# Kernel tuning notes

Hardware: AMD Instinct MI355X
Metric: run time of the kernel (lower is better)

Reference implementation:

```python
import jax, jax.numpy as jnp
import numpy as np

B, Nc, Ns, Nz, Nx, K = 2, 128, 2048, 256, 256, 4


def setup_inputs() -> dict:
    key = jax.random.key(0)
    k1, k2, k3 = jax.random.split(key, 3)
    # RF channel data: [B, Nc, Ns, K]
    rf = jax.random.normal(k1, (B, Nc, Ns, K), dtype=jnp.float32)
    # Imaging grid point coordinates (meters), ~4 cm field: [B, Nz, Nx, 3]
    g = jax.random.uniform(k2, (B, Nz, Nx, 3), dtype=jnp.float32) * 0.04
    # Receiver element positions (meters): [B, Nc, 3]
    pr = jax.random.uniform(k3, (B, Nc, 3), dtype=jnp.float32) * 0.04
    # Acquisition params per batch: [c0 (m/s), fs (Hz), t0 (s), unused]
    p = jnp.tile(jnp.array([1540.0, 40.0e6, 0.0, 0.0], dtype=jnp.float32), (B, 1))
    return {"rf": rf, "g": g, "pr": pr, "p": p}


def reference(rf, g, pr, p):
    # rf: [B, Nc, Ns, K]; g: [B, Nz, Nx, 3]; pr: [B, Nc, 3]; p: [B, 4]
    b, nc, ns, k = rf.shape
    nz, nx = g.shape[1], g.shape[2]
    m = nz * nx

    c0 = p[:, 0][:, None, None, None]
    fs = p[:, 1][:, None, None, None]
    t0 = p[:, 2][:, None, None, None]

    d_tx = g[..., 2]  # [B, Nz, Nx] transmit path = depth coordinate
    # receive path: distance from each receiver to each pixel -> [B, Nc, Nz, Nx]
    d_rx = jnp.linalg.norm(g[:, None, :, :, :] - pr[:, :, None, None, :], axis=-1)
    # fractional sample index of the round-trip delay
    samples = fs * (t0 + (d_rx + d_tx[:, None, :, :])) / c0  # [B, Nc, Nz, Nx]
    s = samples.reshape(b, nc, m)

    # batch_interp_regular_1d_grid with x_ref_min=0, x_ref_max=Ns-1 on Ns points
    # -> unit grid spacing, constant extension (clamp) outside the grid.
    s = jnp.clip(s, 0.0, float(ns - 1))
    i0 = jnp.clip(jnp.floor(s).astype(jnp.int32), 0, ns - 2)  # [B, Nc, M]
    w = (s - i0.astype(s.dtype))[..., None]                   # [B, Nc, M, 1]

    idx0 = jnp.broadcast_to(i0[..., None], (b, nc, m, k))
    y0 = jnp.take_along_axis(rf, idx0, axis=2)      # [B, Nc, M, K]
    y1 = jnp.take_along_axis(rf, idx0 + 1, axis=2)  # [B, Nc, M, K]
    interp = y0 * (1.0 - w) + y1 * w

    # delay-and-sum over channels, then back to image layout [B, Nz, Nx, K]
    y_das = jnp.sum(interp, axis=1).reshape(b, nz, nx, k)
    return y_das
```

## Files before the change

### kernel.cpp

```cpp
#include <hip/hip_runtime.h>


#define NBATCH 2
#define NC 128
#define NS 2048
#define NK 4
#define NM 65536

#define THREADS 1024
#define PX_PER_THREAD 2
#define PX_PER_BLOCK (THREADS * PX_PER_THREAD)
#define C_PER_BLOCK 16
#define N_CHUNKS (NC / C_PER_BLOCK)
#define N_TILES (NM / PX_PER_BLOCK)
#define NBLOCKS (NBATCH * N_TILES * N_CHUNKS)
#define SLICE_F4 (NS * NK / 4)

#define PART_BYTES ((size_t)N_CHUNKS * NBATCH * NM * NK * 4)

__device__ __forceinline__ void stage_channel(const float* slice, float4* lbuf, int t) {
#pragma unroll
    for (int r = 0; r < SLICE_F4 / THREADS; ++r) {
        const int d = r * THREADS + t;
        __builtin_amdgcn_global_load_lds(
            (const __attribute__((address_space(1))) void*)(slice + (size_t)d * 4),
            (__attribute__((address_space(3))) void*)(lbuf + d),
            16, 0, 0);
    }
}

template <bool ATOMIC>
__global__ __launch_bounds__(THREADS, 8) void das_kernel(
    const float* __restrict__ rf, const float* __restrict__ g,
    const float* __restrict__ pr, const float* __restrict__ p,
    float* __restrict__ dst)
{
    __shared__ float4 sbuf[2][SLICE_F4];

    const int bid   = blockIdx.x;
    const int chunk = bid & (N_CHUNKS - 1);
    const int tile  = (bid >> 3) & (N_TILES - 1);
    const int b     = bid >> 8;
    const int t     = threadIdx.x;
    const int px0   = tile * PX_PER_BLOCK;

    const float c0v = p[b * 4 + 0];
    const float fsv = p[b * 4 + 1];
    const float t0v = p[b * 4 + 2];
    const float scale = fsv / c0v;
    const float sb0   = scale * t0v;

    float gx[PX_PER_THREAD], gy[PX_PER_THREAD], gzv[PX_PER_THREAD], sbase[PX_PER_THREAD];
#pragma unroll
    for (int j = 0; j < PX_PER_THREAD; ++j) {
        const int m = px0 + j * THREADS + t;
        const float* gp = g + ((size_t)b * NM + m) * 3;
        gx[j]  = gp[0];
        gy[j]  = gp[1];
        gzv[j] = gp[2];
        sbase[j] = sb0 + scale * gzv[j];
    }

    float4 acc[PX_PER_THREAD];
#pragma unroll
    for (int j = 0; j < PX_PER_THREAD; ++j) acc[j] = make_float4(0.f, 0.f, 0.f, 0.f);

    const int ch0 = chunk * C_PER_BLOCK;
    const float* slice0 = rf + (size_t)(b * NC + ch0) * NS * NK;

    stage_channel(slice0, &sbuf[0][0], t);

    for (int cc = 0; cc < C_PER_BLOCK; ++cc) {
        __syncthreads();
        if (cc + 1 < C_PER_BLOCK)
            stage_channel(slice0 + (size_t)(cc + 1) * NS * NK,
                          &sbuf[(cc + 1) & 1][0], t);

        const float4* lb = &sbuf[cc & 1][0];
        const float* prp = pr + ((size_t)(b * NC + ch0 + cc)) * 3;
        const float prx = prp[0], pry = prp[1], prz = prp[2];

#pragma unroll
        for (int j = 0; j < PX_PER_THREAD; ++j) {
            const float dx = gx[j]  - prx;
            const float dy = gy[j]  - pry;
            const float dz = gzv[j] - prz;
            const float drx = __builtin_amdgcn_sqrtf(fmaf(dx, dx, fmaf(dy, dy, dz * dz)));
            float s = fmaf(scale, drx, sbase[j]);
            s = fminf(fmaxf(s, 0.0f), (float)(NS - 1));
            const float fi = fminf(floorf(s), (float)(NS - 2));
            const float w  = s - fi;
            const float wm = 1.0f - w;
            const int i0 = (int)fi;
            const float4 y0 = lb[i0];
            const float4 y1 = lb[i0 + 1];
            acc[j].x = fmaf(y0.x, wm, fmaf(y1.x, w, acc[j].x));
            acc[j].y = fmaf(y0.y, wm, fmaf(y1.y, w, acc[j].y));
            acc[j].z = fmaf(y0.z, wm, fmaf(y1.z, w, acc[j].z));
            acc[j].w = fmaf(y0.w, wm, fmaf(y1.w, w, acc[j].w));
        }
    }

    if (ATOMIC) {
        float* ob = dst + (size_t)b * NM * NK;
#pragma unroll
        for (int j = 0; j < PX_PER_THREAD; ++j) {
            const int m = px0 + j * THREADS + t;
            float* op = ob + (size_t)m * NK;
            atomicAdd(op + 0, acc[j].x);
            atomicAdd(op + 1, acc[j].y);
            atomicAdd(op + 2, acc[j].z);
            atomicAdd(op + 3, acc[j].w);
        }
    } else {
        float4* pw = (float4*)dst + (size_t)(chunk * NBATCH + b) * NM;
#pragma unroll
        for (int j = 0; j < PX_PER_THREAD; ++j) {
            const int m = px0 + j * THREADS + t;
            pw[m] = acc[j];
        }
    }
}

__global__ __launch_bounds__(256) void reduce_kernel(
    const float4* __restrict__ part, float4* __restrict__ out)
{
    const int i = blockIdx.x * 256 + threadIdx.x;
    const size_t stride = (size_t)NBATCH * NM;
    float4 a = part[i];
#pragma unroll
    for (int c = 1; c < N_CHUNKS; ++c) {
        const float4 v = part[c * stride + i];
        a.x += v.x; a.y += v.y; a.z += v.z; a.w += v.w;
    }
    out[i] = a;
}

extern "C" void kernel_launch(void* const* d_in, const int* in_sizes, int n_in,
                              void* d_out, int out_size, void* d_ws, size_t ws_size,
                              hipStream_t stream) {
    (void)in_sizes; (void)n_in;
    const float* rf = (const float*)d_in[0];
    const float* g  = (const float*)d_in[1];
    const float* pr = (const float*)d_in[2];
    const float* p  = (const float*)d_in[3];
    float* out = (float*)d_out;

    if (ws_size >= PART_BYTES) {
        das_kernel<false><<<NBLOCKS, THREADS, 0, stream>>>(rf, g, pr, p, (float*)d_ws);
        reduce_kernel<<<(NBATCH * NM) / 256, 256, 0, stream>>>((const float4*)d_ws,
                                                               (float4*)out);
    } else {
        hipMemsetAsync(d_out, 0, (size_t)out_size * sizeof(float), stream);
        das_kernel<true><<<NBLOCKS, THREADS, 0, stream>>>(rf, g, pr, p, out);
    }
}
```

Before: 87.58 us.

## Convert RF data to fp16 in a prepass and stage half-size slices

```diff
diff --git a/kernel.cpp b/kernel.cpp
--- a/kernel.cpp
+++ b/kernel.cpp
@@ -1,4 +1,5 @@
 #include <hip/hip_runtime.h>
+#include <hip/hip_fp16.h>
 
 
 #define NBATCH 2
@@ -14,28 +15,35 @@
 #define N_CHUNKS (NC / C_PER_BLOCK)
 #define N_TILES (NM / PX_PER_BLOCK)
 #define NBLOCKS (NBATCH * N_TILES * N_CHUNKS)
-#define SLICE_F4 (NS * NK / 4)
 
 #define PART_BYTES ((size_t)N_CHUNKS * NBATCH * NM * NK * 4)
-
-__device__ __forceinline__ void stage_channel(const float* slice, float4* lbuf, int t) {
-#pragma unroll
-    for (int r = 0; r < SLICE_F4 / THREADS; ++r) {
-        const int d = r * THREADS + t;
-        __builtin_amdgcn_global_load_lds(
-            (const __attribute__((address_space(1))) void*)(slice + (size_t)d * 4),
-            (__attribute__((address_space(3))) void*)(lbuf + d),
-            16, 0, 0);
-    }
-}
-
-template <bool ATOMIC>
-__global__ __launch_bounds__(THREADS, 8) void das_kernel(
-    const float* __restrict__ rf, const float* __restrict__ g,
+#define RF16_BYTES ((size_t)NBATCH * NC * NS * NK * 2)
+#define N_SAMPLES (NBATCH * NC * NS)
+
+__global__ __launch_bounds__(256) void convert_kernel(
+    const float4* __restrict__ rf, uint2* __restrict__ out)
+{
+    const int i = blockIdx.x * 256 + threadIdx.x;
+    const float4 v = rf[i];
+    const __half2 lo = __floats2half2_rn(v.x, v.y);
+    const __half2 hi = __floats2half2_rn(v.z, v.w);
+    out[i] = make_uint2(__builtin_bit_cast(unsigned, lo),
+                        __builtin_bit_cast(unsigned, hi));
+}
+
+__device__ __forceinline__ void stage_channel16(const uint2* slice, uint2* lbuf, int t) {
+    __builtin_amdgcn_global_load_lds(
+        (const __attribute__((address_space(1))) void*)(slice + 2 * t),
+        (__attribute__((address_space(3))) void*)(lbuf + 2 * t),
+        16, 0, 0);
+}
+
+__global__ __launch_bounds__(THREADS, 8) void das16_kernel(
+    const uint2* __restrict__ rf16, const float* __restrict__ g,
     const float* __restrict__ pr, const float* __restrict__ p,
-    float* __restrict__ dst)
-{
-    __shared__ float4 sbuf[2][SLICE_F4];
+    float* __restrict__ part)
+{
+    __shared__ uint2 sbuf[2][NS];
 
     const int bid   = blockIdx.x;
     const int chunk = bid & (N_CHUNKS - 1);
@@ -66,15 +74,109 @@
     for (int j = 0; j < PX_PER_THREAD; ++j) acc[j] = make_float4(0.f, 0.f, 0.f, 0.f);
 
     const int ch0 = chunk * C_PER_BLOCK;
-    const float* slice0 = rf + (size_t)(b * NC + ch0) * NS * NK;
-
-    stage_channel(slice0, &sbuf[0][0], t);
+    const uint2* slice0 = rf16 + (size_t)(b * NC + ch0) * NS;
+
+    stage_channel16(slice0, &sbuf[0][0], t);
 
     for (int cc = 0; cc < C_PER_BLOCK; ++cc) {
         __syncthreads();
         if (cc + 1 < C_PER_BLOCK)
-            stage_channel(slice0 + (size_t)(cc + 1) * NS * NK,
-                          &sbuf[(cc + 1) & 1][0], t);
+            stage_channel16(slice0 + (size_t)(cc + 1) * NS,
+                            &sbuf[(cc + 1) & 1][0], t);
+
+        const uint2* lb = &sbuf[cc & 1][0];
+        const float* prp = pr + ((size_t)(b * NC + ch0 + cc)) * 3;
+        const float prx = prp[0], pry = prp[1], prz = prp[2];
+
+#pragma unroll
+        for (int j = 0; j < PX_PER_THREAD; ++j) {
+            const float dx = gx[j]  - prx;
+            const float dy = gy[j]  - pry;
+            const float dz = gzv[j] - prz;
+            const float drx = __builtin_amdgcn_sqrtf(fmaf(dx, dx, fmaf(dy, dy, dz * dz)));
+            float s = fmaf(scale, drx, sbase[j]);
+            s = fminf(fmaxf(s, 0.0f), (float)(NS - 1));
+            const float fi = fminf(floorf(s), (float)(NS - 2));
+            const float w  = s - fi;
+            const float wm = 1.0f - w;
+            const int i0 = (int)fi;
+            const uint2 u0 = lb[i0];
+            const uint2 u1 = lb[i0 + 1];
+            const float2 y0a = __half22float2(__builtin_bit_cast(__half2, u0.x));
+            const float2 y0b = __half22float2(__builtin_bit_cast(__half2, u0.y));
+            const float2 y1a = __half22float2(__builtin_bit_cast(__half2, u1.x));
+            const float2 y1b = __half22float2(__builtin_bit_cast(__half2, u1.y));
+            acc[j].x = fmaf(y0a.x, wm, fmaf(y1a.x, w, acc[j].x));
+            acc[j].y = fmaf(y0a.y, wm, fmaf(y1a.y, w, acc[j].y));
+            acc[j].z = fmaf(y0b.x, wm, fmaf(y1b.x, w, acc[j].z));
+            acc[j].w = fmaf(y0b.y, wm, fmaf(y1b.y, w, acc[j].w));
+        }
+    }
+
+    float4* pw = (float4*)part + (size_t)(chunk * NBATCH + b) * NM;
+#pragma unroll
+    for (int j = 0; j < PX_PER_THREAD; ++j) {
+        const int m = px0 + j * THREADS + t;
+        pw[m] = acc[j];
+    }
+}
+
+__device__ __forceinline__ void stage_channel32(const float* slice, float4* lbuf, int t) {
+#pragma unroll
+    for (int r = 0; r < (NS * NK / 4) / THREADS; ++r) {
+        const int d = r * THREADS + t;
+        __builtin_amdgcn_global_load_lds(
+            (const __attribute__((address_space(1))) void*)(slice + (size_t)d * 4),
+            (__attribute__((address_space(3))) void*)(lbuf + d),
+            16, 0, 0);
+    }
+}
+
+__global__ __launch_bounds__(THREADS, 8) void das32_atomic_kernel(
+    const float* __restrict__ rf, const float* __restrict__ g,
+    const float* __restrict__ pr, const float* __restrict__ p,
+    float* __restrict__ out)
+{
+    __shared__ float4 sbuf[2][NS * NK / 4];
+
+    const int bid   = blockIdx.x;
+    const int chunk = bid & (N_CHUNKS - 1);
+    const int tile  = (bid >> 3) & (N_TILES - 1);
+    const int b     = bid >> 8;
+    const int t     = threadIdx.x;
+    const int px0   = tile * PX_PER_BLOCK;
+
+    const float c0v = p[b * 4 + 0];
+    const float fsv = p[b * 4 + 1];
+    const float t0v = p[b * 4 + 2];
+    const float scale = fsv / c0v;
+    const float sb0   = scale * t0v;
+
+    float gx[PX_PER_THREAD], gy[PX_PER_THREAD], gzv[PX_PER_THREAD], sbase[PX_PER_THREAD];
+#pragma unroll
+    for (int j = 0; j < PX_PER_THREAD; ++j) {
+        const int m = px0 + j * THREADS + t;
+        const float* gp = g + ((size_t)b * NM + m) * 3;
+        gx[j]  = gp[0];
+        gy[j]  = gp[1];
+        gzv[j] = gp[2];
+        sbase[j] = sb0 + scale * gzv[j];
+    }
+
+    float4 acc[PX_PER_THREAD];
+#pragma unroll
+    for (int j = 0; j < PX_PER_THREAD; ++j) acc[j] = make_float4(0.f, 0.f, 0.f, 0.f);
+
+    const int ch0 = chunk * C_PER_BLOCK;
+    const float* slice0 = rf + (size_t)(b * NC + ch0) * NS * NK;
+
+    stage_channel32(slice0, &sbuf[0][0], t);
+
+    for (int cc = 0; cc < C_PER_BLOCK; ++cc) {
+        __syncthreads();
+        if (cc + 1 < C_PER_BLOCK)
+            stage_channel32(slice0 + (size_t)(cc + 1) * NS * NK,
+                            &sbuf[(cc + 1) & 1][0], t);
 
         const float4* lb = &sbuf[cc & 1][0];
         const float* prp = pr + ((size_t)(b * NC + ch0 + cc)) * 3;
@@ -101,24 +203,15 @@
         }
     }
 
-    if (ATOMIC) {
-        float* ob = dst + (size_t)b * NM * NK;
-#pragma unroll
-        for (int j = 0; j < PX_PER_THREAD; ++j) {
-            const int m = px0 + j * THREADS + t;
-            float* op = ob + (size_t)m * NK;
-            atomicAdd(op + 0, acc[j].x);
-            atomicAdd(op + 1, acc[j].y);
-            atomicAdd(op + 2, acc[j].z);
-            atomicAdd(op + 3, acc[j].w);
-        }
-    } else {
-        float4* pw = (float4*)dst + (size_t)(chunk * NBATCH + b) * NM;
-#pragma unroll
-        for (int j = 0; j < PX_PER_THREAD; ++j) {
-            const int m = px0 + j * THREADS + t;
-            pw[m] = acc[j];
-        }
+    float* ob = out + (size_t)b * NM * NK;
+#pragma unroll
+    for (int j = 0; j < PX_PER_THREAD; ++j) {
+        const int m = px0 + j * THREADS + t;
+        float* op = ob + (size_t)m * NK;
+        atomicAdd(op + 0, acc[j].x);
+        atomicAdd(op + 1, acc[j].y);
+        atomicAdd(op + 2, acc[j].z);
+        atomicAdd(op + 3, acc[j].w);
     }
 }
 
@@ -146,12 +239,14 @@
     const float* p  = (const float*)d_in[3];
     float* out = (float*)d_out;
 
-    if (ws_size >= PART_BYTES) {
-        das_kernel<false><<<NBLOCKS, THREADS, 0, stream>>>(rf, g, pr, p, (float*)d_ws);
+    if (ws_size >= PART_BYTES + RF16_BYTES) {
+        uint2* rf16 = (uint2*)((char*)d_ws + PART_BYTES);
+        convert_kernel<<<N_SAMPLES / 256, 256, 0, stream>>>((const float4*)rf, rf16);
+        das16_kernel<<<NBLOCKS, THREADS, 0, stream>>>(rf16, g, pr, p, (float*)d_ws);
         reduce_kernel<<<(NBATCH * NM) / 256, 256, 0, stream>>>((const float4*)d_ws,
                                                                (float4*)out);
     } else {
         hipMemsetAsync(d_out, 0, (size_t)out_size * sizeof(float), stream);
-        das_kernel<true><<<NBLOCKS, THREADS, 0, stream>>>(rf, g, pr, p, out);
-    }
-}
+        das32_atomic_kernel<<<NBLOCKS, THREADS, 0, stream>>>(rf, g, pr, p, out);
+    }
+}
```

New measurement: 148.0 us. 1.69x slower.
